# Kernel tuning notes

Hardware: AMD Instinct MI355X
Metric: run time of the kernel (lower is better)

The kernel has to match this reference:

```python
import jax, jax.numpy as jnp
import numpy as np

B, N, H, NH = 8, 1024, 512, 8
HD = H // NH
SCALE = float(np.sqrt(HD))


def setup_inputs() -> dict:
    key = jax.random.key(0)
    ks = jax.random.split(key, 14)
    s = 0.02
    return {
        "x": jax.random.normal(ks[0], (B, N, H), jnp.float32),
        "distance_matrix": jax.random.uniform(ks[1], (B, N, N), jnp.float32),
        "mask": jax.random.randint(ks[2], (B, N), 0, 2).astype(bool),
        "Wq": jax.random.normal(ks[3], (H, H), jnp.float32) * s,
        "bq": jnp.zeros((H,), jnp.float32),
        "Wk": jax.random.normal(ks[4], (H, H), jnp.float32) * s,
        "bk": jnp.zeros((H,), jnp.float32),
        "Wv": jax.random.normal(ks[5], (H, H), jnp.float32) * s,
        "bv": jnp.zeros((H,), jnp.float32),
        "Wo": jax.random.normal(ks[6], (H, H), jnp.float32) * s,
        "bo": jnp.zeros((H,), jnp.float32),
        "dist_emb": jax.random.normal(ks[7], (50, NH), jnp.float32) * s,
        "attn_bias": jnp.zeros((NH, 1, 1), jnp.float32),
    }


def reference(x, distance_matrix, mask, Wq, bq, Wk, bk, Wv, bv, Wo, bo, dist_emb, attn_bias):
    Bb, Nn, _ = x.shape
    # projections (torch Linear: x @ W.T + b), split heads -> [B, N, NH, HD]
    Q = (x @ Wq.T + bq).reshape(Bb, Nn, NH, HD)
    K = (x @ Wk.T + bk).reshape(Bb, Nn, NH, HD)
    V = (x @ Wv.T + bv).reshape(Bb, Nn, NH, HD)
    # scores [B, NH, N, N]
    scores = jnp.einsum('bqhd,bkhd->bhqk', Q, K) / SCALE
    # distance-bin bias lookup: [B,N,N] -> bins -> [B,N,N,NH] -> [B,NH,N,N]
    bins = jnp.clip((distance_matrix * 10.0).astype(jnp.int32), 0, 49)
    dbias = jnp.transpose(dist_emb[bins], (0, 3, 1, 2))
    scores = scores + dbias + attn_bias[None]  # attn_bias [NH,1,1] broadcasts
    scores = jnp.where(mask[:, None, None, :], -1e9, scores)  # mask over keys
    attn = jax.nn.softmax(scores, axis=-1)  # dropout = identity in eval
    out = jnp.einsum('bhqk,bkhd->bqhd', attn, V).reshape(Bb, Nn, H)
    return out @ Wo.T + bo
```

## Files before the change

### kernel.cpp

```cpp
#include <hip/hip_runtime.h>
#include <hip/hip_bf16.h>
#include <math.h>

#define B_  8
#define N_  1024
#define H_  512
#define NH_ 8
#define HD_ 64

typedef __attribute__((ext_vector_type(8))) short short8;
typedef __attribute__((ext_vector_type(4))) short short4_t;
typedef __attribute__((ext_vector_type(4))) float floatx4;

#define GPTR(p) ((const __attribute__((address_space(1))) void*)(p))
#define LPTR(p) ((__attribute__((address_space(3))) void*)(p))

#define TRB16(dst, addr, IMM) \
    asm volatile("ds_read_b64_tr_b16 %0, %1 offset:" IMM \
                 : "=v"(dst) : "v"(addr) : "memory")

#define EXP2(x) exp2f(x)
#define LOG2E 1.44269504088896f

static __device__ __forceinline__ unsigned short f2bf(float f) {
    __hip_bfloat16 h = __float2bfloat16(f);
    unsigned short u;
    __builtin_memcpy(&u, &h, 2);
    return u;
}

__global__ __launch_bounds__(256) void prep_kernel(
    const float* __restrict__ x,  const float* __restrict__ wq,
    const float* __restrict__ wk, const float* __restrict__ wv,
    const float* __restrict__ wo, unsigned short* __restrict__ dst,
    const float* __restrict__ dist, const int* __restrict__ mask,
    unsigned char* __restrict__ bins)
{
    const int bid = blockIdx.x;
    if (bid < 1280) {
        const int n4 = (4194304 + 4 * 262144) / 4;
        int i = bid * 256 + threadIdx.x;
        for (; i < n4; i += 1280 * 256) {
            const int e = i * 4;
            const float* src;
            if (e < 4194304) {
                src = x + e;
            } else {
                const int rel = e - 4194304;
                const int w = rel >> 18;
                const int off = rel & 262143;
                src = (w == 0 ? wq : w == 1 ? wk : w == 2 ? wv : wo) + off;
            }
            const float4 v = *(const float4*)src;
            ushort4 r;
            r.x = f2bf(v.x); r.y = f2bf(v.y); r.z = f2bf(v.z); r.w = f2bf(v.w);
            *(ushort4*)(dst + e) = r;
        }
    } else {
        const int gid = (bid - 1280) * 256 + threadIdx.x;
        const size_t e = (size_t)gid * 16;
        const int b = gid >> 16;
        const int k = (gid & 63) * 16;
        const float* dsrc = dist + e;
        const int*   msrc = mask + b * N_ + k;
        unsigned w[4];
        #pragma unroll
        for (int i = 0; i < 4; ++i) {
            const float4 v = *(const float4*)(dsrc + 4 * i);
            const int4  mm = *(const int4*)(msrc + 4 * i);
            int b0 = (int)(v.x * 10.f); b0 = b0 < 0 ? 0 : (b0 > 49 ? 49 : b0);
            int b1 = (int)(v.y * 10.f); b1 = b1 < 0 ? 0 : (b1 > 49 ? 49 : b1);
            int b2 = (int)(v.z * 10.f); b2 = b2 < 0 ? 0 : (b2 > 49 ? 49 : b2);
            int b3 = (int)(v.w * 10.f); b3 = b3 < 0 ? 0 : (b3 > 49 ? 49 : b3);
            if (mm.x) b0 = 255;
            if (mm.y) b1 = 255;
            if (mm.z) b2 = 255;
            if (mm.w) b3 = 255;
            w[i] = (unsigned)b0 | ((unsigned)b1 << 8) | ((unsigned)b2 << 16) | ((unsigned)b3 << 24);
        }
        uint4 u; u.x = w[0]; u.y = w[1]; u.z = w[2]; u.w = w[3];
        *(uint4*)(bins + e) = u;
    }
}

template <int BF16OUT>
static __device__ __forceinline__ void gemm_core(
    const unsigned short* __restrict__ A, const unsigned short* __restrict__ W,
    const float* __restrict__ bias, void* __restrict__ C,
    int Ncols, int K, float scale, int row0, int col0)
{
    __shared__ unsigned short As[128 * 32];
    __shared__ unsigned short Bs[128 * 32];

    const int t    = threadIdx.x;
    const int lane = t & 63;
    const int wave = t >> 6;
    const int wr   = wave >> 1;
    const int wc   = wave & 1;
    const int l15  = lane & 15;
    const int lhi  = lane >> 4;

    const int srow = wave * 32 + (lane >> 2);
    const int sk   = (lane & 3) * 8;
    const unsigned short* gA = A + (size_t)(row0 + srow) * K + sk;
    const unsigned short* gB = W + (size_t)(col0 + srow) * K + sk;

    floatx4 acc[4][4];
    #pragma unroll
    for (int m = 0; m < 4; ++m)
        #pragma unroll
        for (int n = 0; n < 4; ++n) acc[m][n] = (floatx4)0.f;

    for (int k0 = 0; k0 < K; k0 += 32) {
        __syncthreads();
        #pragma unroll
        for (int i = 0; i < 2; ++i) {
            __builtin_amdgcn_global_load_lds(GPTR(gA + (size_t)(i * 16) * K + k0),
                                             LPTR(&As[(wave * 32 + i * 16) * 32]), 16, 0, 0);
            __builtin_amdgcn_global_load_lds(GPTR(gB + (size_t)(i * 16) * K + k0),
                                             LPTR(&Bs[(wave * 32 + i * 16) * 32]), 16, 0, 0);
        }
        __syncthreads();

        short8 af[4], bf[4];
        #pragma unroll
        for (int m = 0; m < 4; ++m)
            af[m] = *(const short8*)&As[(wr * 64 + m * 16 + l15) * 32 + lhi * 8];
        #pragma unroll
        for (int n = 0; n < 4; ++n)
            bf[n] = *(const short8*)&Bs[(wc * 64 + n * 16 + l15) * 32 + lhi * 8];
        #pragma unroll
        for (int m = 0; m < 4; ++m)
            #pragma unroll
            for (int n = 0; n < 4; ++n)
                acc[m][n] = __builtin_amdgcn_mfma_f32_16x16x32_bf16(af[m], bf[n], acc[m][n], 0, 0, 0);
    }

    #pragma unroll
    for (int n = 0; n < 4; ++n) {
        const int col = col0 + wc * 64 + n * 16 + l15;
        const float bvv = bias[col];
        #pragma unroll
        for (int m = 0; m < 4; ++m) {
            #pragma unroll
            for (int r = 0; r < 4; ++r) {
                const int row = row0 + wr * 64 + m * 16 + lhi * 4 + r;
                const float v = (acc[m][n][r] + bvv) * scale;
                if (BF16OUT)
                    ((unsigned short*)C)[(size_t)row * Ncols + col] = f2bf(v);
                else
                    ((float*)C)[(size_t)row * Ncols + col] = v;
            }
        }
    }
}

__global__ __launch_bounds__(256) void gemm_qkv(
    const unsigned short* __restrict__ xb,
    const unsigned short* __restrict__ Wq, const unsigned short* __restrict__ Wk,
    const unsigned short* __restrict__ Wv,
    const float* __restrict__ bq, const float* __restrict__ bk,
    const float* __restrict__ bv,
    unsigned short* __restrict__ Qb, unsigned short* __restrict__ Kb,
    unsigned short* __restrict__ Vb)
{
    const int z = blockIdx.z;
    const unsigned short* W = z == 0 ? Wq : (z == 1 ? Wk : Wv);
    const float* bias       = z == 0 ? bq : (z == 1 ? bk : bv);
    unsigned short* C       = z == 0 ? Qb : (z == 1 ? Kb : Vb);
    const float scale       = z == 0 ? (0.125f * LOG2E) : 1.0f;
    gemm_core<1>(xb, W, bias, C, H_, H_, scale, blockIdx.y * 128, blockIdx.x * 128);
}

__global__ __launch_bounds__(256) void gemm_out(
    const unsigned short* __restrict__ Ab, const unsigned short* __restrict__ Wo,
    const float* __restrict__ bo, float* __restrict__ out)
{
    gemm_core<0>(Ab, Wo, bo, out, H_, H_, 1.0f, blockIdx.y * 128, blockIdx.x * 128);
}

__global__ __launch_bounds__(512) void attn_mfma(
    const unsigned short* __restrict__ Qg, const unsigned short* __restrict__ Kg,
    const unsigned short* __restrict__ Vg, const unsigned char* __restrict__ bins,
    const float* __restrict__ demb, const float* __restrict__ abias,
    unsigned short* __restrict__ O)
{
    const int lin = blockIdx.x + 8 * blockIdx.y + 64 * blockIdx.z;
    const int swz = (lin & 7) * 64 + (lin >> 3);
    const int qt = swz & 7;
    const int h  = (swz >> 3) & 7;
    const int b  = swz >> 6;
    const int q0 = qt * 128;
    const int t  = threadIdx.x;
    const int lane = t & 63;
    const int wave = t >> 6;
    const int l15 = lane & 15;
    const int lhi = lane >> 4;

    __shared__ unsigned short Ks[64 * 64];
    __shared__ unsigned short Vs[64 * 64];
    __shared__ unsigned short QPs[128 * 64];
    __shared__ unsigned char  Bs[128 * 80];

    float dbl = -1.442695e9f;
    if (lane < 50) dbl = (demb[lane * NH_ + h] + abias[h]) * LOG2E;

    const int C = wave * 64 + lane;
    const int kr = C >> 3, kc = C & 7;
    const unsigned short* ksrc =
        Kg + ((size_t)(b * N_) + kr) * H_ + h * HD_ + ((kc ^ (kr & 7)) * 8);
    const int vd16 = C >> 7, vrem = C & 127;
    const int vkrhi = vrem >> 3, vr2 = vrem & 7;
    const int vkr = vkrhi * 4 + (vr2 >> 1), vcc = vr2 & 1;
    const unsigned short* vsrc =
        Vg + ((size_t)(b * N_) + vkr) * H_ + h * HD_ + vd16 * 16 + vcc * 8;
    const unsigned char* bsrc = bins + ((size_t)(b * N_) + q0 + (t >> 2)) * N_ + (t & 3) * 16;
    const int bidx = (t >> 2) * 80 + (t & 3) * 16;

    {
        const int qr = t >> 2;
        const int d0 = (t & 3) * 16;
        const unsigned short* src = Qg + ((size_t)(b * N_ + q0 + qr)) * H_ + h * HD_ + d0;
        #pragma unroll
        for (int cc = 0; cc < 2; ++cc) {
            const uint4 v = *(const uint4*)(src + 8 * cc);
            const int idx = (qr * 64 + d0 + 8 * cc) ^ ((qr & 7) << 3);
            *(uint4*)&QPs[idx] = v;
        }
    }
    __syncthreads();

    short8 aq[2];
    {
        const int qrow = (wave << 4) + l15;
        #pragma unroll
        for (int ck = 0; ck < 2; ++ck) {
            const int kb = lhi * 8 + 32 * ck;
            const int idx = (qrow * 64 + kb) ^ ((qrow & 7) << 3);
            aq[ck] = *(const short8*)&QPs[idx];
        }
    }
    __syncthreads();

    unsigned short* const Pw = &QPs[wave << 10];
    const unsigned trlane = (unsigned)(lhi << 8) + (unsigned)(l15 << 3);
    const unsigned vaddr = (unsigned)(size_t)LPTR(&Vs[0]) + trlane;

    float m = -INFINITY, lsum = 0.f;
    floatx4 o4[4];
    #pragma unroll
    for (int nd = 0; nd < 4; ++nd) o4[nd] = (floatx4)0.f;

    for (int k0 = 0; k0 < N_; k0 += 64) {
        __syncthreads();
        {
            const size_t koff = (size_t)k0;
            __builtin_amdgcn_global_load_lds(GPTR(ksrc + koff * H_),
                LPTR(&Ks[(wave * 64) * 8]), 16, 0, 0);
            __builtin_amdgcn_global_load_lds(GPTR(vsrc + koff * H_),
                LPTR(&Vs[(wave * 64) * 8]), 16, 0, 0);
            const uint4 brv = *(const uint4*)(bsrc + koff);
            *(uint4*)&Bs[bidx] = brv;
        }
        __syncthreads();

        floatx4 s4[4];
        __builtin_amdgcn_s_setprio(1);
        #pragma unroll
        for (int kn = 0; kn < 4; ++kn) {
            const int kcol = kn * 16 + l15;
            floatx4 acc = (floatx4)0.f;
            #pragma unroll
            for (int ck = 0; ck < 2; ++ck) {
                const int kb = lhi * 8 + 32 * ck;
                const int idx = (kcol * 64 + kb) ^ ((kcol & 7) << 3);
                const short8 bk = *(const short8*)&Ks[idx];
                acc = __builtin_amdgcn_mfma_f32_16x16x32_bf16(bk, aq[ck], acc, 0, 0, 0);
            }
            s4[kn] = acc;
        }
        __builtin_amdgcn_s_setprio(0);

        #pragma unroll
        for (int kn = 0; kn < 4; ++kn) {
            const unsigned bb =
                *(const unsigned*)&Bs[((wave << 4) + l15) * 80 + kn * 16 + (lhi << 2)];
            s4[kn][0] += __shfl(dbl, (int)(bb & 255u), 64);
            s4[kn][1] += __shfl(dbl, (int)((bb >> 8) & 255u), 64);
            s4[kn][2] += __shfl(dbl, (int)((bb >> 16) & 255u), 64);
            s4[kn][3] += __shfl(dbl, (int)(bb >> 24), 64);
        }

        {
            float mx = s4[0][0];
            #pragma unroll
            for (int kn = 0; kn < 4; ++kn)
                #pragma unroll
                for (int r = 0; r < 4; ++r) mx = fmaxf(mx, s4[kn][r]);
            mx = fmaxf(mx, __shfl_xor(mx, 16, 64));
            mx = fmaxf(mx, __shfl_xor(mx, 32, 64));
            const float mnew = fmaxf(m, mx);
            float ts = 0.f;
            #pragma unroll
            for (int kn = 0; kn < 4; ++kn)
                #pragma unroll
                for (int r = 0; r < 4; ++r) {
                    const float p = EXP2(s4[kn][r] - mnew);
                    s4[kn][r] = p;
                    ts += p;
                }
            ts += __shfl_xor(ts, 16, 64);
            ts += __shfl_xor(ts, 32, 64);
            const float alpha = EXP2(m - mnew);
            lsum = lsum * alpha + ts;
            m = mnew;
            #pragma unroll
            for (int r = 0; r < 4; ++r) {
                const float ar = __shfl(alpha, lhi * 4 + r, 64);
                #pragma unroll
                for (int nd = 0; nd < 4; ++nd) o4[nd][r] *= ar;
            }
        }

        #pragma unroll
        for (int kn = 0; kn < 4; ++kn) {
            short4_t pk;
            pk[0] = (short)f2bf(s4[kn][0]);
            pk[1] = (short)f2bf(s4[kn][1]);
            pk[2] = (short)f2bf(s4[kn][2]);
            pk[3] = (short)f2bf(s4[kn][3]);
            const int idx = (l15 * 64 + kn * 16 + (lhi << 2)) ^ ((l15 & 7) << 3);
            *(short4_t*)&Pw[idx] = pk;
        }

        short8 ap[2];
        #pragma unroll
        for (int ck = 0; ck < 2; ++ck) {
            const int idx = (l15 * 64 + ck * 32 + lhi * 8) ^ ((l15 & 7) << 3);
            ap[ck] = *(const short8*)&Pw[idx];
        }
        short4_t v0l[4], v0h[4], v1l[4], v1h[4];
        TRB16(v0l[0], vaddr, "0");    TRB16(v0h[0], vaddr, "128");
        TRB16(v0l[1], vaddr, "2048"); TRB16(v0h[1], vaddr, "2176");
        TRB16(v0l[2], vaddr, "4096"); TRB16(v0h[2], vaddr, "4224");
        TRB16(v0l[3], vaddr, "6144"); TRB16(v0h[3], vaddr, "6272");
        TRB16(v1l[0], vaddr, "1024"); TRB16(v1h[0], vaddr, "1152");
        TRB16(v1l[1], vaddr, "3072"); TRB16(v1h[1], vaddr, "3200");
        TRB16(v1l[2], vaddr, "5120"); TRB16(v1h[2], vaddr, "5248");
        TRB16(v1l[3], vaddr, "7168"); TRB16(v1h[3], vaddr, "7296");
        asm volatile("s_waitcnt lgkmcnt(0)" ::: "memory");
        __builtin_amdgcn_sched_barrier(0);

        __builtin_amdgcn_s_setprio(1);
        #pragma unroll
        for (int nd = 0; nd < 4; ++nd) {
            const short8 bv0 = __builtin_shufflevector(v0l[nd], v0h[nd], 0, 1, 2, 3, 4, 5, 6, 7);
            o4[nd] = __builtin_amdgcn_mfma_f32_16x16x32_bf16(ap[0], bv0, o4[nd], 0, 0, 0);
            const short8 bv1 = __builtin_shufflevector(v1l[nd], v1h[nd], 0, 1, 2, 3, 4, 5, 6, 7);
            o4[nd] = __builtin_amdgcn_mfma_f32_16x16x32_bf16(ap[1], bv1, o4[nd], 0, 0, 0);
        }
        __builtin_amdgcn_s_setprio(0);
    }

    float inv[4];
    #pragma unroll
    for (int r = 0; r < 4; ++r) inv[r] = 1.f / __shfl(lsum, lhi * 4 + r, 64);
    #pragma unroll
    for (int nd = 0; nd < 4; ++nd) {
        const int d = nd * 16 + l15;
        #pragma unroll
        for (int r = 0; r < 4; ++r) {
            const int q = q0 + (wave << 4) + lhi * 4 + r;
            O[((size_t)(b * N_ + q)) * H_ + h * HD_ + d] = f2bf(o4[nd][r] * inv[r]);
        }
    }
}

extern "C" void kernel_launch(void* const* d_in, const int* in_sizes, int n_in,
                              void* d_out, int out_size, void* d_ws, size_t ws_size,
                              hipStream_t stream)
{
    const float* x    = (const float*)d_in[0];
    const float* dist = (const float*)d_in[1];
    const int*   mask = (const int*)d_in[2];
    const float* Wq   = (const float*)d_in[3];
    const float* bq   = (const float*)d_in[4];
    const float* Wk   = (const float*)d_in[5];
    const float* bk   = (const float*)d_in[6];
    const float* Wv   = (const float*)d_in[7];
    const float* bv   = (const float*)d_in[8];
    const float* Wo   = (const float*)d_in[9];
    const float* bo   = (const float*)d_in[10];
    const float* demb = (const float*)d_in[11];
    const float* ab   = (const float*)d_in[12];
    float* out = (float*)d_out;

    const size_t mat = (size_t)B_ * N_ * H_;
    const size_t wsz = (size_t)H_ * H_;

    unsigned short* blob = (unsigned short*)d_ws;
    unsigned short* xb  = blob;
    unsigned short* Wqb = blob + mat;
    unsigned short* Wkb = Wqb + wsz;
    unsigned short* Wvb = Wkb + wsz;
    unsigned short* Wob = Wvb + wsz;
    unsigned short* Qb  = Wob + wsz;
    unsigned short* Kb  = Qb + mat;
    unsigned short* Vb  = Kb + mat;
    unsigned short* Ab  = Vb + mat;
    unsigned char*  binsb = (unsigned char*)(Ab + mat);

    const dim3 blk(256);

    hipLaunchKernelGGL(prep_kernel, dim3(3328), blk, 0, stream,
                       x, Wq, Wk, Wv, Wo, blob, dist, mask, binsb);

    const dim3 qgrid(H_ / 128, (B_ * N_) / 128, 3);
    hipLaunchKernelGGL(gemm_qkv, qgrid, blk, 0, stream,
                       xb, Wqb, Wkb, Wvb, bq, bk, bv, Qb, Kb, Vb);

    const dim3 agrid(N_ / 128, NH_, B_);
    hipLaunchKernelGGL(attn_mfma, agrid, dim3(512), 0, stream,
                       Qb, Kb, Vb, binsb, demb, ab, Ab);

    const dim3 ogrid(H_ / 128, (B_ * N_) / 128, 1);
    hipLaunchKernelGGL(gemm_out, ogrid, blk, 0, stream, Ab, Wob, bo, out);
}
```

Baseline: 103.2 us.

## Double-buffer K/V/bin tiles in LDS to overlap loads with compute

```diff
diff --git a/kernel.cpp b/kernel.cpp
--- a/kernel.cpp
+++ b/kernel.cpp
@@ -197,10 +197,10 @@
     const int l15 = lane & 15;
     const int lhi = lane >> 4;
 
-    __shared__ unsigned short Ks[64 * 64];
-    __shared__ unsigned short Vs[64 * 64];
+    __shared__ unsigned short Ks[2][64 * 64];
+    __shared__ unsigned short Vs[2][64 * 64];
     __shared__ unsigned short QPs[128 * 64];
-    __shared__ unsigned char  Bs[128 * 80];
+    __shared__ unsigned char  Bsh[2][128 * 80];
 
     float dbl = -1.442695e9f;
     if (lane < 50) dbl = (demb[lane * NH_ + h] + abias[h]) * LOG2E;
@@ -228,6 +228,9 @@
             *(uint4*)&QPs[idx] = v;
         }
     }
+    const uint4 br0 = *(const uint4*)bsrc;
+    __builtin_amdgcn_global_load_lds(GPTR(ksrc), LPTR(&Ks[0][(wave * 64) * 8]), 16, 0, 0);
+    __builtin_amdgcn_global_load_lds(GPTR(vsrc), LPTR(&Vs[0][(wave * 64) * 8]), 16, 0, 0);
     __syncthreads();
 
     short8 aq[2];
@@ -240,29 +243,30 @@
             aq[ck] = *(const short8*)&QPs[idx];
         }
     }
+    *(uint4*)&Bsh[0][bidx] = br0;
     __syncthreads();
 
     unsigned short* const Pw = &QPs[wave << 10];
     const unsigned trlane = (unsigned)(lhi << 8) + (unsigned)(l15 << 3);
-    const unsigned vaddr = (unsigned)(size_t)LPTR(&Vs[0]) + trlane;
+    const unsigned vbase = (unsigned)(size_t)LPTR(&Vs[0][0]) + trlane;
 
     float m = -INFINITY, lsum = 0.f;
     floatx4 o4[4];
     #pragma unroll
     for (int nd = 0; nd < 4; ++nd) o4[nd] = (floatx4)0.f;
 
-    for (int k0 = 0; k0 < N_; k0 += 64) {
-        __syncthreads();
-        {
-            const size_t koff = (size_t)k0;
+    int p = 0;
+    for (int tt = 0; tt < 16; ++tt) {
+        uint4 brn;
+        if (tt < 15) {
+            const size_t koff = (size_t)((tt + 1) * 64);
+            brn = *(const uint4*)(bsrc + koff);
             __builtin_amdgcn_global_load_lds(GPTR(ksrc + koff * H_),
-                LPTR(&Ks[(wave * 64) * 8]), 16, 0, 0);
+                LPTR(&Ks[1 - p][(wave * 64) * 8]), 16, 0, 0);
             __builtin_amdgcn_global_load_lds(GPTR(vsrc + koff * H_),
-                LPTR(&Vs[(wave * 64) * 8]), 16, 0, 0);
-            const uint4 brv = *(const uint4*)(bsrc + koff);
-            *(uint4*)&Bs[bidx] = brv;
-        }
-        __syncthreads();
+                LPTR(&Vs[1 - p][(wave * 64) * 8]), 16, 0, 0);
+        }
+        const unsigned short* Kp = &Ks[p][0];
 
         floatx4 s4[4];
         __builtin_amdgcn_s_setprio(1);
@@ -274,7 +278,7 @@
             for (int ck = 0; ck < 2; ++ck) {
                 const int kb = lhi * 8 + 32 * ck;
                 const int idx = (kcol * 64 + kb) ^ ((kcol & 7) << 3);
-                const short8 bk = *(const short8*)&Ks[idx];
+                const short8 bk = *(const short8*)&Kp[idx];
                 acc = __builtin_amdgcn_mfma_f32_16x16x32_bf16(bk, aq[ck], acc, 0, 0, 0);
             }
             s4[kn] = acc;
@@ -284,7 +288,7 @@
         #pragma unroll
         for (int kn = 0; kn < 4; ++kn) {
             const unsigned bb =
-                *(const unsigned*)&Bs[((wave << 4) + l15) * 80 + kn * 16 + (lhi << 2)];
+                *(const unsigned*)&Bsh[p][((wave << 4) + l15) * 80 + kn * 16 + (lhi << 2)];
             s4[kn][0] += __shfl(dbl, (int)(bb & 255u), 64);
             s4[kn][1] += __shfl(dbl, (int)((bb >> 8) & 255u), 64);
             s4[kn][2] += __shfl(dbl, (int)((bb >> 16) & 255u), 64);
@@ -305,9 +309,9 @@
             for (int kn = 0; kn < 4; ++kn)
                 #pragma unroll
                 for (int r = 0; r < 4; ++r) {
-                    const float p = EXP2(s4[kn][r] - mnew);
-                    s4[kn][r] = p;
-                    ts += p;
+                    const float pexp = EXP2(s4[kn][r] - mnew);
+                    s4[kn][r] = pexp;
+                    ts += pexp;
                 }
             ts += __shfl_xor(ts, 16, 64);
             ts += __shfl_xor(ts, 32, 64);
@@ -339,6 +343,7 @@
             const int idx = (l15 * 64 + ck * 32 + lhi * 8) ^ ((l15 & 7) << 3);
             ap[ck] = *(const short8*)&Pw[idx];
         }
+        const unsigned vaddr = vbase + (unsigned)(p * 8192);
         short4_t v0l[4], v0h[4], v1l[4], v1h[4];
         TRB16(v0l[0], vaddr, "0");    TRB16(v0h[0], vaddr, "128");
         TRB16(v0l[1], vaddr, "2048"); TRB16(v0h[1], vaddr, "2176");
@@ -360,6 +365,11 @@
             o4[nd] = __builtin_amdgcn_mfma_f32_16x16x32_bf16(ap[1], bv1, o4[nd], 0, 0, 0);
         }
         __builtin_amdgcn_s_setprio(0);
+
+        if (tt < 15)
+            *(uint4*)&Bsh[1 - p][bidx] = brn;
+        __syncthreads();
+        p ^= 1;
     }
 
     float inv[4];
```

After: 102.2 us, median of 2. About the same (-0.9%).
